# Performance work log

Hardware: AMD Instinct MI355X
Metric: run time of the kernel (lower is better)

Reference implementation:

```python
import jax, jax.numpy as jnp
import numpy as np

N = 4096
IN_F = 512
OUT_F = 128
C = 4            # out_channels
ALPHA = 0.2      # leaky relu slope
P_DROP = 0.6
NEG = -9e15


def setup_inputs() -> dict:
    key = jax.random.key(0)
    k1, k2, k3, k4 = jax.random.split(key, 4)
    x = jax.random.normal(k1, (N, IN_F), dtype=jnp.float32)
    # filter-bank output (Chebyshev spectral filter), non-negative-ish values
    attention = jax.random.uniform(k2, (C * N, N), dtype=jnp.float32)
    drop_mask = jax.random.randint(k3, (C * N, N), 0, 2).astype(bool)
    # nn.Linear(in_features, out_features, bias=False): weight [out_f, in_f]
    W = jax.random.normal(k4, (OUT_F, IN_F), dtype=jnp.float32) / np.sqrt(IN_F)
    return {"x": x, "attention": attention, "W": W, "drop_mask": drop_mask}


def reference(x, attention, W, drop_mask):
    h = x @ W.T                                   # [N, out_f]
    n = h.shape[0]
    overall_mean = attention.mean()
    a = jnp.where(attention > overall_mean, attention, jnp.float32(NEG))
    a = jnp.where(a > 0, a, ALPHA * a)            # LeakyReLU
    a = jax.nn.softmax(a, axis=0)                 # softmax over rows (dim=0)
    a = jnp.where(drop_mask, a / (1.0 - P_DROP), 0.0)  # dropout (training)
    h_prime = a @ h                               # [C*N, out_f]
    # concat=True branch: (C, N, F) -> (N, C, F) -> (N, C*F)
    out = h_prime.reshape(C, n, OUT_F).transpose(1, 0, 2).reshape(n, C * OUT_F)
    return out
```

## Files before the change

### kernel.cpp

```cpp
#include <hip/hip_runtime.h>
#include <stdint.h>

#define KDIM  4096
#define NROWS 16384
#define INF   512
#define OUTF  128

typedef short bf16x8 __attribute__((ext_vector_type(8)));
typedef float f32x4  __attribute__((ext_vector_type(4)));
typedef unsigned short u16;

#define WS_MEAN 0
#define WS_RSZ  16
#define WS_H2P  16400
#define WS_PART 1064976
#define WS_LEAF WS_PART
#define WS_SUB  (WS_PART + 2097152)
#define WS_ZP   (WS_PART + 2099200)
#define PART_STRIDE ((size_t)NROWS*OUTF)

__device__ __forceinline__ u16 f32_to_bf16_rne(float f){
  unsigned u = __float_as_uint(f);
  unsigned r = u + 0x7fffu + ((u >> 16) & 1u);
  return (u16)(r >> 16);
}

__global__ void __launch_bounds__(256) k_leaf(const float* __restrict__ att,
                                              float* __restrict__ leaf){
  int lf = blockIdx.x*256 + threadIdx.x;
  const float* p = att + (size_t)lf*128;
  float4 u = *(const float4*)p;
  float4 v = *(const float4*)(p + 4);
  float c0=u.x, c1=u.y, c2=u.z, c3=u.w, c4=v.x, c5=v.y, c6=v.z, c7=v.w;
  #pragma unroll
  for (int j = 1; j < 16; ++j){
    float4 a = *(const float4*)(p + j*8);
    float4 b = *(const float4*)(p + j*8 + 4);
    c0+=a.x; c1+=a.y; c2+=a.z; c3+=a.w;
    c4+=b.x; c5+=b.y; c6+=b.z; c7+=b.w;
  }
  leaf[lf] = ((c0+c1)+(c2+c3)) + ((c4+c5)+(c6+c7));
}

__global__ void __launch_bounds__(256) k_tree1(const float* __restrict__ leaf,
                                               float* __restrict__ sub){
  __shared__ float A[1024], B[512];
  int b = blockIdx.x;
  for (int i = threadIdx.x; i < 1024; i += 256) A[i] = leaf[(size_t)b*1024 + i];
  __syncthreads();
  for (int i = threadIdx.x; i < 512; i += 256) B[i] = A[2*i] + A[2*i+1];
  __syncthreads();
  if (threadIdx.x < 256) A[threadIdx.x] = B[2*threadIdx.x] + B[2*threadIdx.x+1];
  __syncthreads();
  int n = 128; float* src = A; float* dst = B;
  while (n >= 1){
    if (threadIdx.x < n) dst[threadIdx.x] = src[2*threadIdx.x] + src[2*threadIdx.x+1];
    __syncthreads();
    float* t = src; src = dst; dst = t; n >>= 1;
  }
  if (threadIdx.x == 0) sub[b] = src[0];
}

__global__ void __launch_bounds__(256) k_tree2(const float* __restrict__ sub,
                                               float* __restrict__ meanv){
  __shared__ float A[512], B[256];
  for (int i = threadIdx.x; i < 512; i += 256) A[i] = sub[i];
  __syncthreads();
  int n = 256; float* src = A; float* dst = B;
  while (n >= 1){
    if (threadIdx.x < n) dst[threadIdx.x] = src[2*threadIdx.x] + src[2*threadIdx.x+1];
    __syncthreads();
    float* t = src; src = dst; dst = t; n >>= 1;
  }
  if (threadIdx.x == 0) meanv[0] = src[0] * (1.0f/67108864.0f);
}

__global__ void __launch_bounds__(256) k_zf(const float* __restrict__ att,
                                            const float* __restrict__ meanv,
                                            float* __restrict__ Zp){
  const float mean = meanv[0];
  const int sb = blockIdx.x & 63;
  const int rs = blockIdx.x >> 6;
  const int c8 = threadIdx.x & 7;
  const int r  = threadIdx.x >> 3;
  const int col = sb*64 + c8*8;
  float a0=0.f,a1=0.f,a2=0.f,a3=0.f,a4=0.f,a5=0.f,a6=0.f,a7=0.f;
  #pragma unroll 2
  for (int it = 0; it < 16; ++it){
    int row = rs*512 + it*32 + r;
    const float* p = att + (size_t)row*KDIM + col;
    float4 u = *(const float4*)p;
    float4 v = *(const float4*)(p + 4);
    a0 += (u.x > mean) ? __expf(u.x) : 0.f;
    a1 += (u.y > mean) ? __expf(u.y) : 0.f;
    a2 += (u.z > mean) ? __expf(u.z) : 0.f;
    a3 += (u.w > mean) ? __expf(u.w) : 0.f;
    a4 += (v.x > mean) ? __expf(v.x) : 0.f;
    a5 += (v.y > mean) ? __expf(v.y) : 0.f;
    a6 += (v.z > mean) ? __expf(v.z) : 0.f;
    a7 += (v.w > mean) ? __expf(v.w) : 0.f;
  }
  __shared__ float lds[32][72];
  lds[r][c8*8+0]=a0; lds[r][c8*8+1]=a1; lds[r][c8*8+2]=a2; lds[r][c8*8+3]=a3;
  lds[r][c8*8+4]=a4; lds[r][c8*8+5]=a5; lds[r][c8*8+6]=a6; lds[r][c8*8+7]=a7;
  __syncthreads();
  if (threadIdx.x < 64){
    float s = 0.f;
    #pragma unroll
    for (int rr = 0; rr < 32; ++rr) s += lds[rr][threadIdx.x];
    Zp[(size_t)rs*KDIM + sb*64 + threadIdx.x] = s;
  }
}

__global__ void k_rsz(const float* __restrict__ Zp, float* __restrict__ rsZ){
  int i = blockIdx.x*256 + threadIdx.x;
  if (i < KDIM){
    float s = 0.f;
    #pragma unroll
    for (int rs = 0; rs < 32; ++rs) s += Zp[(size_t)rs*KDIM + i];
    rsZ[i] = 2.5f / s;
  }
}

__device__ __forceinline__ bf16x8 cvt8(float4 a, float4 b){
  bf16x8 r;
  r[0]=(short)f32_to_bf16_rne(a.x); r[1]=(short)f32_to_bf16_rne(a.y);
  r[2]=(short)f32_to_bf16_rne(a.z); r[3]=(short)f32_to_bf16_rne(a.w);
  r[4]=(short)f32_to_bf16_rne(b.x); r[5]=(short)f32_to_bf16_rne(b.y);
  r[6]=(short)f32_to_bf16_rne(b.z); r[7]=(short)f32_to_bf16_rne(b.w);
  return r;
}

__global__ void __launch_bounds__(256) k_h(const float* __restrict__ x,
                                           const float* __restrict__ W,
                                           const float* __restrict__ rsZ,
                                           u16* __restrict__ h2p){
  const int wave = threadIdx.x >> 6, l = threadIdx.x & 63;
  const int rt = blockIdx.x*4 + wave;
  const int m = l & 15, q = l >> 4;
  f32x4 acc[8];
  #pragma unroll
  for (int nt = 0; nt < 8; ++nt) acc[nt] = (f32x4){0.f,0.f,0.f,0.f};
  for (int kb = 0; kb < 16; ++kb){
    const float* xp = x + (size_t)(rt*16+m)*INF + kb*32 + q*8;
    bf16x8 af = cvt8(*(const float4*)xp, *(const float4*)(xp+4));
    #pragma unroll
    for (int nt = 0; nt < 8; ++nt){
      const float* wp = W + (size_t)(nt*16+m)*INF + kb*32 + q*8;
      bf16x8 bf = cvt8(*(const float4*)wp, *(const float4*)(wp+4));
      acc[nt] = __builtin_amdgcn_mfma_f32_16x16x32_bf16(af, bf, acc[nt], 0,0,0);
    }
  }
  float4 rz = *(const float4*)(rsZ + rt*16 + q*4);
  float rzv[4] = {rz.x, rz.y, rz.z, rz.w};
  #pragma unroll
  for (int nt = 0; nt < 8; ++nt)
    #pragma unroll
    for (int r = 0; r < 4; ++r){
      int j = rt*16 + q*4 + r;
      int kb2 = j >> 5, lane_t = ((j>>3)&3)*16 + m, ii = j & 7;
      h2p[(size_t)(kb2*8 + nt)*512 + lane_t*8 + ii] =
          f32_to_bf16_rne(acc[nt][r] * rzv[r]);
    }
}

__device__ __forceinline__ bf16x8 make_afrag(float4 fl, float4 fh, int4 ma, int4 mb,
                                             float mean){
  float w0 = (fl.x > mean && ma.x != 0) ? __expf(fl.x) : 0.f;
  float w1 = (fl.y > mean && ma.y != 0) ? __expf(fl.y) : 0.f;
  float w2 = (fl.z > mean && ma.z != 0) ? __expf(fl.z) : 0.f;
  float w3 = (fl.w > mean && ma.w != 0) ? __expf(fl.w) : 0.f;
  float w4 = (fh.x > mean && mb.x != 0) ? __expf(fh.x) : 0.f;
  float w5 = (fh.y > mean && mb.y != 0) ? __expf(fh.y) : 0.f;
  float w6 = (fh.z > mean && mb.z != 0) ? __expf(fh.z) : 0.f;
  float w7 = (fh.w > mean && mb.w != 0) ? __expf(fh.w) : 0.f;
  bf16x8 r;
  r[0]=(short)f32_to_bf16_rne(w0); r[1]=(short)f32_to_bf16_rne(w1);
  r[2]=(short)f32_to_bf16_rne(w2); r[3]=(short)f32_to_bf16_rne(w3);
  r[4]=(short)f32_to_bf16_rne(w4); r[5]=(short)f32_to_bf16_rne(w5);
  r[6]=(short)f32_to_bf16_rne(w6); r[7]=(short)f32_to_bf16_rne(w7);
  return r;
}

template<int S>
__global__ void __launch_bounds__(256,2) k_mm(const float* __restrict__ att,
    const int* __restrict__ mask, const float* __restrict__ meanv,
    const u16* __restrict__ h2p, float* __restrict__ part,
    float* __restrict__ out){
  const float mean = meanv[0];
  const int gw = blockIdx.x*4 + (threadIdx.x >> 6);
  const int rp = gw & 511;
  const int kh = gw >> 9;
  const int l = threadIdx.x & 63, m = l & 15, q = l >> 4;
  const int KB = 128 / S;
  const int kb0 = kh * KB;
  const size_t ro0 = (size_t)(rp*32 + m) * KDIM;
  const size_t ro1 = ro0 + (size_t)16 * KDIM;
  f32x4 acc[2][8];
  #pragma unroll
  for (int rt = 0; rt < 2; ++rt)
    #pragma unroll
    for (int nt = 0; nt < 8; ++nt) acc[rt][nt] = (f32x4){0.f,0.f,0.f,0.f};

  float4 A0l[2], A0h[2], A1l[2], A1h[2];
  int4   M0l[2], M0h[2], M1l[2], M1h[2];
  bf16x8 Bv[2][8];

#define LOADSTAGE(kb_, s_) {                                                  \
    const int kc = (kb_)*32 + q*8;                                            \
    A0l[s_] = *(const float4*)(att + ro0 + kc);                               \
    A0h[s_] = *(const float4*)(att + ro0 + kc + 4);                           \
    A1l[s_] = *(const float4*)(att + ro1 + kc);                               \
    A1h[s_] = *(const float4*)(att + ro1 + kc + 4);                           \
    M0l[s_] = *(const int4*)(mask + ro0 + kc);                                \
    M0h[s_] = *(const int4*)(mask + ro0 + kc + 4);                            \
    M1l[s_] = *(const int4*)(mask + ro1 + kc);                                \
    M1h[s_] = *(const int4*)(mask + ro1 + kc + 4);                            \
    const u16* bp_ = h2p + (size_t)((kb_)*8)*512 + l*8;                       \
    _Pragma("unroll")                                                         \
    for (int nt = 0; nt < 8; ++nt) Bv[s_][nt] = *(const bf16x8*)(bp_ + nt*512); }

#define COMPSTAGE(s_) {                                                       \
    bf16x8 a0 = make_afrag(A0l[s_], A0h[s_], M0l[s_], M0h[s_], mean);         \
    bf16x8 a1 = make_afrag(A1l[s_], A1h[s_], M1l[s_], M1h[s_], mean);         \
    _Pragma("unroll")                                                         \
    for (int nt = 0; nt < 8; ++nt){                                           \
      acc[0][nt] = __builtin_amdgcn_mfma_f32_16x16x32_bf16(a0, Bv[s_][nt], acc[0][nt], 0,0,0); \
      acc[1][nt] = __builtin_amdgcn_mfma_f32_16x16x32_bf16(a1, Bv[s_][nt], acc[1][nt], 0,0,0); } }

  LOADSTAGE(kb0, 0);
  int kb = kb0;
  for (; kb + 2 < kb0 + KB; kb += 2){
    LOADSTAGE(kb+1, 1);
    COMPSTAGE(0);
    LOADSTAGE(kb+2, 0);
    COMPSTAGE(1);
  }
  LOADSTAGE(kb0 + KB - 1, 1);
  COMPSTAGE(0);
  COMPSTAGE(1);
#undef LOADSTAGE
#undef COMPSTAGE

  if (S == 1){
    #pragma unroll
    for (int rt = 0; rt < 2; ++rt)
      #pragma unroll
      for (int nt = 0; nt < 8; ++nt)
        #pragma unroll
        for (int r = 0; r < 4; ++r){
          int i = rp*32 + rt*16 + q*4 + r;
          int f = nt*16 + m;
          out[(size_t)(i & 4095)*512 + (i >> 12)*128 + f] = acc[rt][nt][r];
        }
  } else {
    float* pb = part + (size_t)kh * PART_STRIDE;
    #pragma unroll
    for (int rt = 0; rt < 2; ++rt)
      #pragma unroll
      for (int nt = 0; nt < 8; ++nt)
        #pragma unroll
        for (int r = 0; r < 4; ++r){
          int i = rp*32 + rt*16 + q*4 + r;
          int f = nt*16 + m;
          pb[(size_t)i*128 + f] = acc[rt][nt][r];
        }
  }
}

template<int S>
__global__ void __launch_bounds__(256) k_red(const float* __restrict__ part,
                                             float* __restrict__ out){
  int g = blockIdx.x*256 + threadIdx.x;
  int i = g >> 5;
  int fo = (g & 31) << 2;
  const float* p = part + (size_t)i*128 + fo;
  float4 s = *(const float4*)p;
  #pragma unroll
  for (int kh = 1; kh < S; ++kh){
    float4 t = *(const float4*)(p + (size_t)kh * PART_STRIDE);
    s.x += t.x; s.y += t.y; s.z += t.z; s.w += t.w;
  }
  int n = i & 4095, c = i >> 12;
  *(float4*)(out + (size_t)n*512 + c*128 + fo) = s;
}

extern "C" void kernel_launch(void* const* d_in, const int* in_sizes, int n_in,
                              void* d_out, int out_size, void* d_ws, size_t ws_size,
                              hipStream_t stream) {
  const float* x    = (const float*)d_in[0];
  const float* att  = (const float*)d_in[1];
  const float* W    = (const float*)d_in[2];
  const int*   mask = (const int*)d_in[3];
  float* out = (float*)d_out;

  char* ws = (char*)d_ws;
  float* meanv = (float*)(ws + WS_MEAN);
  float* rsZ   = (float*)(ws + WS_RSZ);
  u16*   h2p   = (u16*)(ws + WS_H2P);
  float* part  = (float*)(ws + WS_PART);
  float* leaf  = (float*)(ws + WS_LEAF);
  float* sub   = (float*)(ws + WS_SUB);
  float* Zp    = (float*)(ws + WS_ZP);

  int S = 1;
  if (ws_size >= (size_t)WS_PART + 4ull*PART_STRIDE*4ull) S = 4;
  else if (ws_size >= (size_t)WS_PART + 2ull*PART_STRIDE*4ull) S = 2;

  k_leaf <<<2048, 256, 0, stream>>>(att, leaf);
  k_tree1<<<512,  256, 0, stream>>>(leaf, sub);
  k_tree2<<<1,    256, 0, stream>>>(sub, meanv);
  k_zf   <<<2048, 256, 0, stream>>>(att, meanv, Zp);
  k_rsz  <<<16,   256, 0, stream>>>(Zp, rsZ);
  k_h    <<<64,   256, 0, stream>>>(x, W, rsZ, h2p);

  switch (S){
    case 4:
      k_mm<4><<<512, 256, 0, stream>>>(att, mask, meanv, h2p, part, out);
      k_red<4><<<2048, 256, 0, stream>>>(part, out);
      break;
    case 2:
      k_mm<2><<<256, 256, 0, stream>>>(att, mask, meanv, h2p, part, out);
      k_red<2><<<2048, 256, 0, stream>>>(part, out);
      break;
    default:
      k_mm<1><<<128, 256, 0, stream>>>(att, mask, meanv, h2p, part, out);
      break;
  }
}
```

Baseline: 727.7 us.

## Precompute masked exp weights as bf16 in column-sum pass, stream them in matmul

```diff
diff --git a/kernel.cpp b/kernel.cpp
--- a/kernel.cpp
+++ b/kernel.cpp
@@ -13,7 +13,8 @@
 #define WS_MEAN 0
 #define WS_RSZ  16
 #define WS_H2P  16400
-#define WS_PART 1064976
+#define WS_W    1064976
+#define WS_PART 135282704
 #define WS_LEAF WS_PART
 #define WS_SUB  (WS_PART + 2097152)
 #define WS_ZP   (WS_PART + 2099200)
@@ -75,9 +76,11 @@
   if (threadIdx.x == 0) meanv[0] = src[0] * (1.0f/67108864.0f);
 }
 
-__global__ void __launch_bounds__(256) k_zf(const float* __restrict__ att,
-                                            const float* __restrict__ meanv,
-                                            float* __restrict__ Zp){
+__global__ void __launch_bounds__(256) k_w(const float* __restrict__ att,
+                                           const int* __restrict__ mask,
+                                           const float* __restrict__ meanv,
+                                           u16* __restrict__ w,
+                                           float* __restrict__ Zp){
   const float mean = meanv[0];
   const int sb = blockIdx.x & 63;
   const int rs = blockIdx.x >> 6;
@@ -89,16 +92,30 @@
   for (int it = 0; it < 16; ++it){
     int row = rs*512 + it*32 + r;
     const float* p = att + (size_t)row*KDIM + col;
+    const int*   q = mask + (size_t)row*KDIM + col;
     float4 u = *(const float4*)p;
     float4 v = *(const float4*)(p + 4);
-    a0 += (u.x > mean) ? __expf(u.x) : 0.f;
-    a1 += (u.y > mean) ? __expf(u.y) : 0.f;
-    a2 += (u.z > mean) ? __expf(u.z) : 0.f;
-    a3 += (u.w > mean) ? __expf(u.w) : 0.f;
-    a4 += (v.x > mean) ? __expf(v.x) : 0.f;
-    a5 += (v.y > mean) ? __expf(v.y) : 0.f;
-    a6 += (v.z > mean) ? __expf(v.z) : 0.f;
-    a7 += (v.w > mean) ? __expf(v.w) : 0.f;
+    int4 mu = *(const int4*)q;
+    int4 mv = *(const int4*)(q + 4);
+    float e0 = (u.x > mean) ? __expf(u.x) : 0.f;
+    float e1 = (u.y > mean) ? __expf(u.y) : 0.f;
+    float e2 = (u.z > mean) ? __expf(u.z) : 0.f;
+    float e3 = (u.w > mean) ? __expf(u.w) : 0.f;
+    float e4 = (v.x > mean) ? __expf(v.x) : 0.f;
+    float e5 = (v.y > mean) ? __expf(v.y) : 0.f;
+    float e6 = (v.z > mean) ? __expf(v.z) : 0.f;
+    float e7 = (v.w > mean) ? __expf(v.w) : 0.f;
+    a0+=e0; a1+=e1; a2+=e2; a3+=e3; a4+=e4; a5+=e5; a6+=e6; a7+=e7;
+    bf16x8 wv;
+    wv[0]=(short)f32_to_bf16_rne(mu.x ? e0 : 0.f);
+    wv[1]=(short)f32_to_bf16_rne(mu.y ? e1 : 0.f);
+    wv[2]=(short)f32_to_bf16_rne(mu.z ? e2 : 0.f);
+    wv[3]=(short)f32_to_bf16_rne(mu.w ? e3 : 0.f);
+    wv[4]=(short)f32_to_bf16_rne(mv.x ? e4 : 0.f);
+    wv[5]=(short)f32_to_bf16_rne(mv.y ? e5 : 0.f);
+    wv[6]=(short)f32_to_bf16_rne(mv.z ? e6 : 0.f);
+    wv[7]=(short)f32_to_bf16_rne(mv.w ? e7 : 0.f);
+    *(bf16x8*)(w + (size_t)row*KDIM + col) = wv;
   }
   __shared__ float lds[32][72];
   lds[r][c8*8+0]=a0; lds[r][c8*8+1]=a1; lds[r][c8*8+2]=a2; lds[r][c8*8+3]=a3;
@@ -164,30 +181,10 @@
     }
 }
 
-__device__ __forceinline__ bf16x8 make_afrag(float4 fl, float4 fh, int4 ma, int4 mb,
-                                             float mean){
-  float w0 = (fl.x > mean && ma.x != 0) ? __expf(fl.x) : 0.f;
-  float w1 = (fl.y > mean && ma.y != 0) ? __expf(fl.y) : 0.f;
-  float w2 = (fl.z > mean && ma.z != 0) ? __expf(fl.z) : 0.f;
-  float w3 = (fl.w > mean && ma.w != 0) ? __expf(fl.w) : 0.f;
-  float w4 = (fh.x > mean && mb.x != 0) ? __expf(fh.x) : 0.f;
-  float w5 = (fh.y > mean && mb.y != 0) ? __expf(fh.y) : 0.f;
-  float w6 = (fh.z > mean && mb.z != 0) ? __expf(fh.z) : 0.f;
-  float w7 = (fh.w > mean && mb.w != 0) ? __expf(fh.w) : 0.f;
-  bf16x8 r;
-  r[0]=(short)f32_to_bf16_rne(w0); r[1]=(short)f32_to_bf16_rne(w1);
-  r[2]=(short)f32_to_bf16_rne(w2); r[3]=(short)f32_to_bf16_rne(w3);
-  r[4]=(short)f32_to_bf16_rne(w4); r[5]=(short)f32_to_bf16_rne(w5);
-  r[6]=(short)f32_to_bf16_rne(w6); r[7]=(short)f32_to_bf16_rne(w7);
-  return r;
-}
-
 template<int S>
-__global__ void __launch_bounds__(256,2) k_mm(const float* __restrict__ att,
-    const int* __restrict__ mask, const float* __restrict__ meanv,
+__global__ void __launch_bounds__(256,2) k_mm(const u16* __restrict__ w,
     const u16* __restrict__ h2p, float* __restrict__ part,
     float* __restrict__ out){
-  const float mean = meanv[0];
   const int gw = blockIdx.x*4 + (threadIdx.x >> 6);
   const int rp = gw & 511;
   const int kh = gw >> 9;
@@ -202,31 +199,22 @@
     #pragma unroll
     for (int nt = 0; nt < 8; ++nt) acc[rt][nt] = (f32x4){0.f,0.f,0.f,0.f};
 
-  float4 A0l[2], A0h[2], A1l[2], A1h[2];
-  int4   M0l[2], M0h[2], M1l[2], M1h[2];
+  bf16x8 Aw0[2], Aw1[2];
   bf16x8 Bv[2][8];
 
 #define LOADSTAGE(kb_, s_) {                                                  \
     const int kc = (kb_)*32 + q*8;                                            \
-    A0l[s_] = *(const float4*)(att + ro0 + kc);                               \
-    A0h[s_] = *(const float4*)(att + ro0 + kc + 4);                           \
-    A1l[s_] = *(const float4*)(att + ro1 + kc);                               \
-    A1h[s_] = *(const float4*)(att + ro1 + kc + 4);                           \
-    M0l[s_] = *(const int4*)(mask + ro0 + kc);                                \
-    M0h[s_] = *(const int4*)(mask + ro0 + kc + 4);                            \
-    M1l[s_] = *(const int4*)(mask + ro1 + kc);                                \
-    M1h[s_] = *(const int4*)(mask + ro1 + kc + 4);                            \
+    Aw0[s_] = *(const bf16x8*)(w + ro0 + kc);                                 \
+    Aw1[s_] = *(const bf16x8*)(w + ro1 + kc);                                 \
     const u16* bp_ = h2p + (size_t)((kb_)*8)*512 + l*8;                       \
     _Pragma("unroll")                                                         \
     for (int nt = 0; nt < 8; ++nt) Bv[s_][nt] = *(const bf16x8*)(bp_ + nt*512); }
 
 #define COMPSTAGE(s_) {                                                       \
-    bf16x8 a0 = make_afrag(A0l[s_], A0h[s_], M0l[s_], M0h[s_], mean);         \
-    bf16x8 a1 = make_afrag(A1l[s_], A1h[s_], M1l[s_], M1h[s_], mean);         \
     _Pragma("unroll")                                                         \
     for (int nt = 0; nt < 8; ++nt){                                           \
-      acc[0][nt] = __builtin_amdgcn_mfma_f32_16x16x32_bf16(a0, Bv[s_][nt], acc[0][nt], 0,0,0); \
-      acc[1][nt] = __builtin_amdgcn_mfma_f32_16x16x32_bf16(a1, Bv[s_][nt], acc[1][nt], 0,0,0); } }
+      acc[0][nt] = __builtin_amdgcn_mfma_f32_16x16x32_bf16(Aw0[s_], Bv[s_][nt], acc[0][nt], 0,0,0); \
+      acc[1][nt] = __builtin_amdgcn_mfma_f32_16x16x32_bf16(Aw1[s_], Bv[s_][nt], acc[1][nt], 0,0,0); } }
 
   LOADSTAGE(kb0, 0);
   int kb = kb0;
@@ -298,33 +286,34 @@
   float* meanv = (float*)(ws + WS_MEAN);
   float* rsZ   = (float*)(ws + WS_RSZ);
   u16*   h2p   = (u16*)(ws + WS_H2P);
+  u16*   wbuf  = (u16*)(ws + WS_W);
   float* part  = (float*)(ws + WS_PART);
   float* leaf  = (float*)(ws + WS_LEAF);
   float* sub   = (float*)(ws + WS_SUB);
   float* Zp    = (float*)(ws + WS_ZP);
 
   int S = 1;
-  if (ws_size >= (size_t)WS_PART + 4ull*PART_STRIDE*4ull) S = 4;
-  else if (ws_size >= (size_t)WS_PART + 2ull*PART_STRIDE*4ull) S = 2;
+  if (ws_size >= (size_t)WS_PART + 8ull*PART_STRIDE*4ull) S = 8;
+  else if (ws_size >= (size_t)WS_PART + 4ull*PART_STRIDE*4ull) S = 4;
 
   k_leaf <<<2048, 256, 0, stream>>>(att, leaf);
   k_tree1<<<512,  256, 0, stream>>>(leaf, sub);
   k_tree2<<<1,    256, 0, stream>>>(sub, meanv);
-  k_zf   <<<2048, 256, 0, stream>>>(att, meanv, Zp);
+  k_w    <<<2048, 256, 0, stream>>>(att, mask, meanv, wbuf, Zp);
   k_rsz  <<<16,   256, 0, stream>>>(Zp, rsZ);
   k_h    <<<64,   256, 0, stream>>>(x, W, rsZ, h2p);
 
   switch (S){
+    case 8:
+      k_mm<8><<<1024, 256, 0, stream>>>(wbuf, h2p, part, out);
+      k_red<8><<<2048, 256, 0, stream>>>(part, out);
+      break;
     case 4:
-      k_mm<4><<<512, 256, 0, stream>>>(att, mask, meanv, h2p, part, out);
+      k_mm<4><<<512, 256, 0, stream>>>(wbuf, h2p, part, out);
       k_red<4><<<2048, 256, 0, stream>>>(part, out);
       break;
-    case 2:
-      k_mm<2><<<256, 256, 0, stream>>>(att, mask, meanv, h2p, part, out);
-      k_red<2><<<2048, 256, 0, stream>>>(part, out);
+    default:
+      k_mm<1><<<128, 256, 0, stream>>>(wbuf, h2p, part, out);
       break;
-    default:
-      k_mm<1><<<128, 256, 0, stream>>>(att, mask, meanv, h2p, part, out);
-      break;
-  }
-}
+  }
+}
```

New measurement: 800.3 us. 10.0% more time.
